# Kernel tuning notes

Measured on AMD Instinct MI355X. Metric: run time of the kernel, lower is better.

The kernel has to match this reference:

```python
import jax, jax.numpy as jnp
import numpy as np

N = 100000   # nodes
E = 1600000  # edges
DIN = 128
HID = 128
D2 = 64      # hard-coded last-conv width in the module
OUT = 1000


def setup_inputs() -> dict:
    key = jax.random.key(0)
    ks = jax.random.split(key, 8)
    x = jax.random.normal(ks[0], (N, DIN), dtype=jnp.float32)
    edge_index = jax.random.randint(ks[1], (2, E), 0, N, dtype=jnp.int64)
    W1 = jax.random.normal(ks[2], (DIN, HID), dtype=jnp.float32) * 0.05
    b1 = jnp.zeros((HID,), dtype=jnp.float32)
    W2 = jax.random.normal(ks[3], (HID, D2), dtype=jnp.float32) * 0.05
    b2 = jnp.zeros((D2,), dtype=jnp.float32)
    Wfc = jax.random.normal(ks[4], (D2, OUT), dtype=jnp.float32) * 0.05
    bfc = jnp.zeros((OUT,), dtype=jnp.float32)
    return {"x": x, "W1": W1, "b1": b1, "W2": W2, "b2": b2,
            "Wfc": Wfc, "bfc": bfc, "edge_index": edge_index}


def _gcn_conv(x, W, b, src, dst):
    # PyG GCNConv: h = X W; add self-loops; symmetric norm D^-1/2 (A+I) D^-1/2; + bias
    h = x @ W                                   # [N, F]
    ones = jnp.ones(src.shape[0], dtype=h.dtype)
    deg = jax.ops.segment_sum(ones, dst, num_segments=N) + 1.0  # +1 for self-loop
    dinv = jax.lax.rsqrt(deg)                   # [N]
    norm = dinv[src] * dinv[dst]                # [E]
    agg = jax.ops.segment_sum(h[src] * norm[:, None], dst, num_segments=N)
    agg = agg + h * (dinv * dinv)[:, None]      # self-loop contribution
    return agg + b


def reference(x, W1, b1, W2, b2, Wfc, bfc, edge_index):
    src, dst = edge_index[0], edge_index[1]
    h = jax.nn.relu(_gcn_conv(x, W1, b1, src, dst))
    # dropout is identity in eval mode (training=False)
    h = jax.nn.relu(_gcn_conv(h, W2, b2, src, dst))
    return h @ Wfc + bfc
```

## Files before the change

### kernel.cpp

```cpp
#include <hip/hip_runtime.h>
#include <hip/hip_bf16.h>
#include <cstddef>

typedef __attribute__((ext_vector_type(8))) short bf16x8;
typedef __attribute__((ext_vector_type(4))) float f32x4;

__device__ __forceinline__ unsigned short f2bf(float f) {
    __hip_bfloat16 h = __float2bfloat16(f);
    return __builtin_bit_cast(unsigned short, h);
}
__device__ __forceinline__ float bf2f(unsigned short u) {
    return __bfloat162float(__builtin_bit_cast(__hip_bfloat16, u));
}


__global__ void k_zero_i(int* __restrict__ p, int total) {
    int i = blockIdx.x * blockDim.x + threadIdx.x;
    int stride = gridDim.x * blockDim.x;
    for (; i < total; i += stride) p[i] = 0;
}


__global__ void k_deg_i(const int* __restrict__ dst, int* __restrict__ deg, int E) {
    int e = blockIdx.x * blockDim.x + threadIdx.x;
    if (e < E) atomicAdd(&deg[dst[e]], 1);
}

__global__ void k_dinv(const int* __restrict__ deg, float* __restrict__ dinv, int N) {
    int i = blockIdx.x * blockDim.x + threadIdx.x;
    if (i < N) dinv[i] = rsqrtf((float)deg[i] + 1.0f);
}


#define SCAN_B 1024

__global__ void k_scan1(const int* __restrict__ in, int* __restrict__ out,
                        int* __restrict__ sums, int n) {
    __shared__ int tmp[SCAN_B];
    int tid = threadIdx.x;
    int gid = blockIdx.x * SCAN_B + tid;
    int v = (gid < n) ? in[gid] : 0;
    tmp[tid] = v;
    __syncthreads();
    for (int off = 1; off < SCAN_B; off <<= 1) {
        int t = (tid >= off) ? tmp[tid - off] : 0;
        __syncthreads();
        tmp[tid] += t;
        __syncthreads();
    }
    if (gid < n) out[gid] = tmp[tid] - v;
    if (tid == SCAN_B - 1) sums[blockIdx.x] = tmp[tid];
}

__global__ void k_scan2(int* __restrict__ sums, int nb) {
    __shared__ int tmp[128];
    int tid = threadIdx.x;
    int v = (tid < nb) ? sums[tid] : 0;
    tmp[tid] = v;
    __syncthreads();
    for (int off = 1; off < 128; off <<= 1) {
        int t = (tid >= off) ? tmp[tid - off] : 0;
        __syncthreads();
        tmp[tid] += t;
        __syncthreads();
    }
    if (tid < nb) sums[tid] = tmp[tid] - v;
}

__global__ void k_scan3(int* __restrict__ out, int* __restrict__ cursor,
                        const int* __restrict__ sums, int n) {
    int gid = blockIdx.x * SCAN_B + threadIdx.x;
    if (gid < n) {
        int v = out[gid] + sums[blockIdx.x];
        out[gid] = v;
        cursor[gid] = v;
    }
}


__global__ void k_fill(const int* __restrict__ src, const int* __restrict__ dst,
                       int* __restrict__ cursor, int* __restrict__ csr_src, int E) {
    int e = blockIdx.x * blockDim.x + threadIdx.x;
    if (e < E) {
        int pos = atomicAdd(&cursor[dst[e]], 1);
        csr_src[pos] = src[e];
    }
}


__global__ void k_conv_w(const float* __restrict__ W, unsigned short* __restrict__ Bh,
                         unsigned short* __restrict__ Bl, int K, int N)
{
    int n = blockIdx.x;
    int k = threadIdx.x;
    float v = W[(size_t)k * N + n];
    unsigned short hi = f2bf(v);
    unsigned short lo = f2bf(v - bf2f(hi));
    Bh[(size_t)n * K + k] = hi;
    Bl[(size_t)n * K + k] = lo;
}


__device__ __forceinline__ float4 shfl_xor4(float4 v, int m) {
    return make_float4(__shfl_xor(v.x, m), __shfl_xor(v.y, m),
                       __shfl_xor(v.z, m), __shfl_xor(v.w, m));
}

__device__ __forceinline__ void fmaa4(float4& c, float w, const float4& v) {
    c.x = fmaf(w, v.x, c.x);
    c.y = fmaf(w, v.y, c.y);
    c.z = fmaf(w, v.z, c.z);
    c.w = fmaf(w, v.w, c.w);
}


__launch_bounds__(256)
__global__ void k_gather128(const float* __restrict__ h, const int* __restrict__ csr_src,
                            const int* __restrict__ off, const float* __restrict__ dinv,
                            const float* __restrict__ bias,
                            unsigned short* __restrict__ ohi, unsigned short* __restrict__ olo,
                            int N, int E)
{
    int node = blockIdx.x * 4 + (threadIdx.x >> 6);
    int lane = threadIdx.x & 63;
    if (node >= N) return;
    float dn = dinv[node];
    int beg = off[node];
    int end = (node + 1 < N) ? off[node + 1] : E;

    const int grp = lane >> 5;
    const int sub = lane & 31;

    float4 acc = make_float4(0.f, 0.f, 0.f, 0.f);
    int i = beg + grp;
    for (; i + 6 < end; i += 8) {
        int s0 = csr_src[i];
        int s1 = csr_src[i + 2];
        int s2 = csr_src[i + 4];
        int s3 = csr_src[i + 6];
        float w0 = dinv[s0] * dn;
        float w1 = dinv[s1] * dn;
        float w2 = dinv[s2] * dn;
        float w3 = dinv[s3] * dn;
        float4 v0 = *(const float4*)(h + (size_t)s0 * 128 + sub * 4);
        float4 v1 = *(const float4*)(h + (size_t)s1 * 128 + sub * 4);
        float4 v2 = *(const float4*)(h + (size_t)s2 * 128 + sub * 4);
        float4 v3 = *(const float4*)(h + (size_t)s3 * 128 + sub * 4);
        fmaa4(acc, w0, v0);
        fmaa4(acc, w1, v1);
        fmaa4(acc, w2, v2);
        fmaa4(acc, w3, v3);
    }
    for (; i < end; i += 2) {
        int s = csr_src[i];
        float w = dinv[s] * dn;
        float4 v = *(const float4*)(h + (size_t)s * 128 + sub * 4);
        fmaa4(acc, w, v);
    }
    {
        float4 o = shfl_xor4(acc, 32);
        acc.x += o.x; acc.y += o.y; acc.z += o.z; acc.w += o.w;
    }
    if (grp == 0) {
        float4 hv = *(const float4*)(h + (size_t)node * 128 + sub * 4);
        float4 bv = *(const float4*)(bias + sub * 4);
        float w = dn * dn;
        float f0 = fmaxf(fmaf(hv.x, w, acc.x) + bv.x, 0.f);
        float f1 = fmaxf(fmaf(hv.y, w, acc.y) + bv.y, 0.f);
        float f2 = fmaxf(fmaf(hv.z, w, acc.z) + bv.z, 0.f);
        float f3 = fmaxf(fmaf(hv.w, w, acc.w) + bv.w, 0.f);
        ushort4 hi, lo;
        hi.x = f2bf(f0); lo.x = f2bf(f0 - bf2f(hi.x));
        hi.y = f2bf(f1); lo.y = f2bf(f1 - bf2f(hi.y));
        hi.z = f2bf(f2); lo.z = f2bf(f2 - bf2f(hi.z));
        hi.w = f2bf(f3); lo.w = f2bf(f3 - bf2f(hi.w));
        *(ushort4*)(ohi + (size_t)node * 128 + sub * 4) = hi;
        *(ushort4*)(olo + (size_t)node * 128 + sub * 4) = lo;
    }
}


__launch_bounds__(256)
__global__ void k_gather64(const float* __restrict__ h, const int* __restrict__ csr_src,
                           const int* __restrict__ off, const float* __restrict__ dinv,
                           const float* __restrict__ bias,
                           unsigned short* __restrict__ hhi, unsigned short* __restrict__ hlo,
                           int N, int E)
{
    int node = blockIdx.x * 4 + (threadIdx.x >> 6);
    int lane = threadIdx.x & 63;
    if (node >= N) return;
    float dn = dinv[node];
    int beg = off[node];
    int end = (node + 1 < N) ? off[node + 1] : E;

    const int grp = lane >> 4;
    const int sub = lane & 15;

    float4 acc = make_float4(0.f, 0.f, 0.f, 0.f);
    int i = beg + grp;
    for (; i + 4 < end; i += 8) {
        int s0 = csr_src[i];
        int s1 = csr_src[i + 4];
        float w0 = dinv[s0] * dn;
        float w1 = dinv[s1] * dn;
        float4 v0 = *(const float4*)(h + (size_t)s0 * 64 + sub * 4);
        float4 v1 = *(const float4*)(h + (size_t)s1 * 64 + sub * 4);
        fmaa4(acc, w0, v0);
        fmaa4(acc, w1, v1);
    }
    if (i < end) {
        int s = csr_src[i];
        float w = dinv[s] * dn;
        float4 v = *(const float4*)(h + (size_t)s * 64 + sub * 4);
        fmaa4(acc, w, v);
    }
    acc = make_float4(acc.x + __shfl_xor(acc.x, 16),
                      acc.y + __shfl_xor(acc.y, 16),
                      acc.z + __shfl_xor(acc.z, 16),
                      acc.w + __shfl_xor(acc.w, 16));
    {
        float4 o = shfl_xor4(acc, 32);
        acc.x += o.x; acc.y += o.y; acc.z += o.z; acc.w += o.w;
    }
    if (grp == 0) {
        float4 hv = *(const float4*)(h + (size_t)node * 64 + sub * 4);
        float4 bv = *(const float4*)(bias + sub * 4);
        float w = dn * dn;
        float f0 = fmaxf(fmaf(hv.x, w, acc.x) + bv.x, 0.f);
        float f1 = fmaxf(fmaf(hv.y, w, acc.y) + bv.y, 0.f);
        float f2 = fmaxf(fmaf(hv.z, w, acc.z) + bv.z, 0.f);
        float f3 = fmaxf(fmaf(hv.w, w, acc.w) + bv.w, 0.f);
        ushort4 hi, lo;
        hi.x = f2bf(f0); lo.x = f2bf(f0 - bf2f(hi.x));
        hi.y = f2bf(f1); lo.y = f2bf(f1 - bf2f(hi.y));
        hi.z = f2bf(f2); lo.z = f2bf(f2 - bf2f(hi.z));
        hi.w = f2bf(f3); lo.w = f2bf(f3 - bf2f(hi.w));
        *(ushort4*)(hhi + (size_t)node * 64 + sub * 4) = hi;
        *(ushort4*)(hlo + (size_t)node * 64 + sub * 4) = lo;
    }
}


__launch_bounds__(256, 2)
__global__ void gemm_mfma_l1(const float* __restrict__ A,
                             const unsigned short* __restrict__ Bth,
                             const unsigned short* __restrict__ Btl,
                             float* __restrict__ C, int M)
{
    __shared__ unsigned short Ah[128 * 64], Al[128 * 64];
    __shared__ unsigned short Bh[128 * 64], Bl[128 * 64];

    const int tid = threadIdx.x;
    const int m0 = blockIdx.x * 128;
    const int lane = tid & 63, wave = tid >> 6;
    const int wr = wave >> 1, wc = wave & 1;
    const int lrow = lane & 15, kgrp = lane >> 4;

    f32x4 acc[4][4] = {};

    for (int ph = 0; ph < 2; ++ph) {
        const int k0 = ph * 64;
        __syncthreads();
        {
            const int c4 = tid & 15, r0 = tid >> 4;
#pragma unroll
            for (int p = 0; p < 8; ++p) {
                int row = r0 + p * 16;
                int gr = m0 + row; if (gr >= M) gr = M - 1;
                float4 v = *(const float4*)(A + (size_t)gr * 128 + k0 + c4 * 4);
                ushort4 hi, lo;
                hi.x = f2bf(v.x); lo.x = f2bf(v.x - bf2f(hi.x));
                hi.y = f2bf(v.y); lo.y = f2bf(v.y - bf2f(hi.y));
                hi.z = f2bf(v.z); lo.z = f2bf(v.z - bf2f(hi.z));
                hi.w = f2bf(v.w); lo.w = f2bf(v.w - bf2f(hi.w));
                int off = row * 128 + ((c4 * 8) ^ ((row & 7) << 4));
                *(ushort4*)((char*)Ah + off) = hi;
                *(ushort4*)((char*)Al + off) = lo;
            }
        }
        {
            const int c = tid & 7, col0 = tid >> 3;
#pragma unroll
            for (int p = 0; p < 4; ++p) {
                int col = col0 + p * 32;
                uint4 v = *(const uint4*)(Bth + (size_t)col * 128 + k0 + c * 8);
                uint4 w = *(const uint4*)(Btl + (size_t)col * 128 + k0 + c * 8);
                int off = col * 128 + ((c * 16) ^ ((col & 7) << 4));
                *(uint4*)((char*)Bh + off) = v;
                *(uint4*)((char*)Bl + off) = w;
            }
        }
        __syncthreads();

#pragma unroll
        for (int ks = 0; ks < 2; ++ks) {
            const int cIdx = kgrp + ks * 4;
            bf16x8 ah[4], al[4], bh[4], bl[4];
#pragma unroll
            for (int i = 0; i < 4; ++i) {
                int row = wr * 64 + i * 16 + lrow;
                int off = row * 128 + ((cIdx * 16) ^ ((row & 7) << 4));
                ah[i] = *(const bf16x8*)((const char*)Ah + off);
                al[i] = *(const bf16x8*)((const char*)Al + off);
            }
#pragma unroll
            for (int j = 0; j < 4; ++j) {
                int col = wc * 64 + j * 16 + lrow;
                int off = col * 128 + ((cIdx * 16) ^ ((col & 7) << 4));
                bh[j] = *(const bf16x8*)((const char*)Bh + off);
                bl[j] = *(const bf16x8*)((const char*)Bl + off);
            }
#pragma unroll
            for (int i = 0; i < 4; ++i)
#pragma unroll
                for (int j = 0; j < 4; ++j) {
                    acc[i][j] = __builtin_amdgcn_mfma_f32_16x16x32_bf16(bh[j], ah[i], acc[i][j], 0, 0, 0);
                    acc[i][j] = __builtin_amdgcn_mfma_f32_16x16x32_bf16(bl[j], ah[i], acc[i][j], 0, 0, 0);
                    acc[i][j] = __builtin_amdgcn_mfma_f32_16x16x32_bf16(bh[j], al[i], acc[i][j], 0, 0, 0);
                }
        }
    }

#pragma unroll
    for (int i = 0; i < 4; ++i) {
        int grow = m0 + wr * 64 + i * 16 + lrow;
        if (grow >= M) continue;
        float* crow = C + (size_t)grow * 128;
#pragma unroll
        for (int j = 0; j < 4; ++j) {
            int gc = wc * 64 + j * 16 + kgrp * 4;
            *(float4*)(crow + gc) = make_float4(acc[i][j][0], acc[i][j][1],
                                                acc[i][j][2], acc[i][j][3]);
        }
    }
}


__launch_bounds__(256, 3)
__global__ void gemm_mfma_l2(const unsigned short* __restrict__ Ahi_g,
                             const unsigned short* __restrict__ Alo_g,
                             const unsigned short* __restrict__ Bth,
                             const unsigned short* __restrict__ Btl,
                             float* __restrict__ C, int M)
{
    __shared__ unsigned short Ah[128 * 64], Al[128 * 64];
    __shared__ unsigned short Bh[64 * 64],  Bl[64 * 64];

    const int tid = threadIdx.x;
    const int m0 = blockIdx.x * 128;
    const int lane = tid & 63, wave = tid >> 6;
    const int wr = wave >> 1, wc = wave & 1;
    const int lrow = lane & 15, kgrp = lane >> 4;

    f32x4 acc[4][2] = {};

    for (int ph = 0; ph < 2; ++ph) {
        const int k0 = ph * 64;
        __syncthreads();
        {
            const int c = tid & 7, r0 = tid >> 3;
#pragma unroll
            for (int p = 0; p < 4; ++p) {
                int row = r0 + p * 32;
                int gr = m0 + row; if (gr >= M) gr = M - 1;
                uint4 v = *(const uint4*)(Ahi_g + (size_t)gr * 128 + k0 + c * 8);
                uint4 w = *(const uint4*)(Alo_g + (size_t)gr * 128 + k0 + c * 8);
                int off = row * 128 + ((c * 16) ^ ((row & 7) << 4));
                *(uint4*)((char*)Ah + off) = v;
                *(uint4*)((char*)Al + off) = w;
            }
        }
        {
            const int c = tid & 7, col0 = tid >> 3;
#pragma unroll
            for (int p = 0; p < 2; ++p) {
                int col = col0 + p * 32;
                uint4 v = *(const uint4*)(Bth + (size_t)col * 128 + k0 + c * 8);
                uint4 w = *(const uint4*)(Btl + (size_t)col * 128 + k0 + c * 8);
                int off = col * 128 + ((c * 16) ^ ((col & 7) << 4));
                *(uint4*)((char*)Bh + off) = v;
                *(uint4*)((char*)Bl + off) = w;
            }
        }
        __syncthreads();

#pragma unroll
        for (int ks = 0; ks < 2; ++ks) {
            const int cIdx = kgrp + ks * 4;
            bf16x8 ah[4], al[4], bh[2], bl[2];
#pragma unroll
            for (int i = 0; i < 4; ++i) {
                int row = wr * 64 + i * 16 + lrow;
                int off = row * 128 + ((cIdx * 16) ^ ((row & 7) << 4));
                ah[i] = *(const bf16x8*)((const char*)Ah + off);
                al[i] = *(const bf16x8*)((const char*)Al + off);
            }
#pragma unroll
            for (int j = 0; j < 2; ++j) {
                int col = wc * 32 + j * 16 + lrow;
                int off = col * 128 + ((cIdx * 16) ^ ((col & 7) << 4));
                bh[j] = *(const bf16x8*)((const char*)Bh + off);
                bl[j] = *(const bf16x8*)((const char*)Bl + off);
            }
#pragma unroll
            for (int i = 0; i < 4; ++i)
#pragma unroll
                for (int j = 0; j < 2; ++j) {
                    acc[i][j] = __builtin_amdgcn_mfma_f32_16x16x32_bf16(bh[j], ah[i], acc[i][j], 0, 0, 0);
                    acc[i][j] = __builtin_amdgcn_mfma_f32_16x16x32_bf16(bl[j], ah[i], acc[i][j], 0, 0, 0);
                    acc[i][j] = __builtin_amdgcn_mfma_f32_16x16x32_bf16(bh[j], al[i], acc[i][j], 0, 0, 0);
                }
        }
    }

#pragma unroll
    for (int i = 0; i < 4; ++i) {
        int grow = m0 + wr * 64 + i * 16 + lrow;
        if (grow >= M) continue;
        float* crow = C + (size_t)grow * 64;
#pragma unroll
        for (int j = 0; j < 2; ++j) {
            int gc = wc * 32 + j * 16 + kgrp * 4;
            *(float4*)(crow + gc) = make_float4(acc[i][j][0], acc[i][j][1],
                                                acc[i][j][2], acc[i][j][3]);
        }
    }
}


__launch_bounds__(256, 2)
__global__ void gemm_mfma_out(const unsigned short* __restrict__ Ahi,
                              const unsigned short* __restrict__ Alo,
                              const unsigned short* __restrict__ Bhi,
                              const unsigned short* __restrict__ Blo,
                              const float* __restrict__ bias, float* __restrict__ C,
                              int M, int N)
{
    const int tid = threadIdx.x;
    const int lane = tid & 63, wave = tid >> 6;
    const int wr = wave >> 1, wc = wave & 1;
    const int m0 = blockIdx.x * 128 + wr * 64;
    const int n0 = blockIdx.y * 128 + wc * 64;
    const int lrow = lane & 15, kgrp = lane >> 4;

    f32x4 acc[4][4] = {};

#pragma unroll
    for (int ks = 0; ks < 2; ++ks) {
        const int koff = (kgrp + ks * 4) * 8;
        bf16x8 ah[4], al[4], bh[4], bl[4];
#pragma unroll
        for (int i = 0; i < 4; ++i) {
            int row = m0 + i * 16 + lrow; if (row >= M) row = M - 1;
            ah[i] = *(const bf16x8*)(Ahi + (size_t)row * 64 + koff);
            al[i] = *(const bf16x8*)(Alo + (size_t)row * 64 + koff);
        }
#pragma unroll
        for (int j = 0; j < 4; ++j) {
            int col = n0 + j * 16 + lrow; if (col >= N) col = N - 1;
            bh[j] = *(const bf16x8*)(Bhi + (size_t)col * 64 + koff);
            bl[j] = *(const bf16x8*)(Blo + (size_t)col * 64 + koff);
        }
#pragma unroll
        for (int i = 0; i < 4; ++i)
#pragma unroll
            for (int j = 0; j < 4; ++j) {
                acc[i][j] = __builtin_amdgcn_mfma_f32_16x16x32_bf16(bh[j], ah[i], acc[i][j], 0, 0, 0);
                acc[i][j] = __builtin_amdgcn_mfma_f32_16x16x32_bf16(bl[j], ah[i], acc[i][j], 0, 0, 0);
                acc[i][j] = __builtin_amdgcn_mfma_f32_16x16x32_bf16(bh[j], al[i], acc[i][j], 0, 0, 0);
            }
    }

#pragma unroll
    for (int i = 0; i < 4; ++i) {
        int grow = m0 + i * 16 + lrow;
        if (grow >= M) continue;
        float* crow = C + (size_t)grow * N;
#pragma unroll
        for (int j = 0; j < 4; ++j) {
            int gc = n0 + j * 16 + kgrp * 4;
            if (gc + 4 <= N) {
                float4 bv = *(const float4*)(bias + gc);
                *(float4*)(crow + gc) = make_float4(acc[i][j][0] + bv.x,
                                                    acc[i][j][1] + bv.y,
                                                    acc[i][j][2] + bv.z,
                                                    acc[i][j][3] + bv.w);
            }
        }
    }
}


extern "C" void kernel_launch(void* const* d_in, const int* in_sizes, int n_in,
                              void* d_out, int out_size, void* d_ws, size_t ws_size,
                              hipStream_t stream)
{
    const float* x   = (const float*)d_in[0];
    const float* W1  = (const float*)d_in[1];
    const float* b1  = (const float*)d_in[2];
    const float* W2  = (const float*)d_in[3];
    const float* b2  = (const float*)d_in[4];
    const float* Wfc = (const float*)d_in[5];
    const float* bfc = (const float*)d_in[6];
    const int*   ei  = (const int*)d_in[7];

    const int Nn = in_sizes[0] / 128;
    const int E  = in_sizes[7] / 2;
    const int* src = ei;
    const int* dst = ei + E;

    char* ws = (char*)d_ws;
    float*          dinv   = (float*)(ws);
    unsigned short* Wfc_hi = (unsigned short*)(ws + 512 * 1024);
    unsigned short* Wfc_lo = (unsigned short*)(ws + 768 * 1024);
    unsigned short* W1_hi  = (unsigned short*)(ws + 1024 * 1024);
    unsigned short* W1_lo  = (unsigned short*)(ws + 1088 * 1024);
    unsigned short* W2_hi  = (unsigned short*)(ws + 1152 * 1024);
    unsigned short* W2_lo  = (unsigned short*)(ws + 1216 * 1024);
    unsigned short* h2hi   = (unsigned short*)(ws + 1280 * 1024);
    unsigned short* h2lo   = (unsigned short*)(ws + 1280 * 1024 + (size_t)Nn * 64 * 2);

    float* out = (float*)d_out;
    float*          O0      = out;
    unsigned short* h1hi    = (unsigned short*)(out + (size_t)Nn * 128);
    unsigned short* h1lo    = (unsigned short*)(out + (size_t)Nn * 192);
    float*          O2      = out + (size_t)Nn * 256;
    int*            csr_src = (int*)(out + (size_t)Nn * 320);
    int*            offs    = (int*)((char*)csr_src + (size_t)E * 4);
    int*            cursor  = (int*)((char*)offs + (size_t)Nn * 4);
    int*            deg_cnt = (int*)((char*)cursor + (size_t)Nn * 4);
    int*            bsums   = (int*)((char*)deg_cnt + (size_t)Nn * 4);

    const int nScanBlocks = (Nn + SCAN_B - 1) / SCAN_B;

    k_zero_i<<<128, 256, 0, stream>>>(deg_cnt, Nn);
    k_deg_i<<<(E + 255) / 256, 256, 0, stream>>>(dst, deg_cnt, E);
    k_dinv<<<(Nn + 255) / 256, 256, 0, stream>>>(deg_cnt, dinv, Nn);
    k_scan1<<<nScanBlocks, SCAN_B, 0, stream>>>(deg_cnt, offs, bsums, Nn);
    k_scan2<<<1, 128, 0, stream>>>(bsums, nScanBlocks);
    k_scan3<<<nScanBlocks, SCAN_B, 0, stream>>>(offs, cursor, bsums, Nn);
    k_fill<<<(E + 255) / 256, 256, 0, stream>>>(src, dst, cursor, csr_src, E);
    k_conv_w<<<128, 128, 0, stream>>>(W1, W1_hi, W1_lo, 128, 128);
    k_conv_w<<<64, 128, 0, stream>>>(W2, W2_hi, W2_lo, 128, 64);
    k_conv_w<<<1000, 64, 0, stream>>>(Wfc, Wfc_hi, Wfc_lo, 64, 1000);

    gemm_mfma_l1<<<dim3((Nn + 127) / 128, 1), 256, 0, stream>>>(x, W1_hi, W1_lo, O0, Nn);
    k_gather128<<<(Nn + 3) / 4, 256, 0, stream>>>(O0, csr_src, offs, dinv, b1,
                                                  h1hi, h1lo, Nn, E);

    gemm_mfma_l2<<<dim3((Nn + 127) / 128, 1), 256, 0, stream>>>(h1hi, h1lo, W2_hi, W2_lo, O2, Nn);
    k_gather64<<<(Nn + 3) / 4, 256, 0, stream>>>(O2, csr_src, offs, dinv, b2,
                                                 h2hi, h2lo, Nn, E);

    gemm_mfma_out<<<dim3((Nn + 127) / 128, (1000 + 127) / 128), 256, 0, stream>>>(
        h2hi, h2lo, Wfc_hi, Wfc_lo, bfc, out, Nn, 1000);
}
```

Before: 606.0 us.

## Store GEMM outputs as bf16 and gather bf16 rows in aggregation kernels

The layer-1 and layer-2 GEMMs now write their XW products as single bf16 values instead of fp32. The gather/aggregation kernels read 8 bf16 elements per lane with uint4 loads, unpack them to fp32 and accumulate, with lane groups and shuffle reductions reworked to match. This halves the bytes moved by the random neighbour gathers, which dominate memory traffic, and by the GEMM stores. In exchange it loses precision on the aggregated features (bf16 rounding of h before the sum), unlike the hi/lo split kept elsewhere.

```diff
diff --git a/kernel.cpp b/kernel.cpp
--- a/kernel.cpp
+++ b/kernel.cpp
@@ -11,6 +11,12 @@
 }
 __device__ __forceinline__ float bf2f(unsigned short u) {
     return __bfloat162float(__builtin_bit_cast(__hip_bfloat16, u));
+}
+__device__ __forceinline__ float bflo(unsigned u) {
+    return __builtin_bit_cast(float, u << 16);
+}
+__device__ __forceinline__ float bfhi(unsigned u) {
+    return __builtin_bit_cast(float, u & 0xffff0000u);
 }
 
 
@@ -101,23 +107,21 @@
 }
 
 
-__device__ __forceinline__ float4 shfl_xor4(float4 v, int m) {
-    return make_float4(__shfl_xor(v.x, m), __shfl_xor(v.y, m),
-                       __shfl_xor(v.z, m), __shfl_xor(v.w, m));
-}
-
-__device__ __forceinline__ void fmaa4(float4& c, float w, const float4& v) {
-    c.x = fmaf(w, v.x, c.x);
-    c.y = fmaf(w, v.y, c.y);
-    c.z = fmaf(w, v.z, c.z);
-    c.w = fmaf(w, v.w, c.w);
-}
-
+__device__ __forceinline__ void unpack_fma(float* a, float w, uint4 v) {
+    a[0] = fmaf(w, bflo(v.x), a[0]);
+    a[1] = fmaf(w, bfhi(v.x), a[1]);
+    a[2] = fmaf(w, bflo(v.y), a[2]);
+    a[3] = fmaf(w, bfhi(v.y), a[3]);
+    a[4] = fmaf(w, bflo(v.z), a[4]);
+    a[5] = fmaf(w, bfhi(v.z), a[5]);
+    a[6] = fmaf(w, bflo(v.w), a[6]);
+    a[7] = fmaf(w, bfhi(v.w), a[7]);
+}
 
 __launch_bounds__(256)
-__global__ void k_gather128(const float* __restrict__ h, const int* __restrict__ csr_src,
-                            const int* __restrict__ off, const float* __restrict__ dinv,
-                            const float* __restrict__ bias,
+__global__ void k_gather128(const unsigned short* __restrict__ hbf,
+                            const int* __restrict__ csr_src, const int* __restrict__ off,
+                            const float* __restrict__ dinv, const float* __restrict__ bias,
                             unsigned short* __restrict__ ohi, unsigned short* __restrict__ olo,
                             int N, int E)
 {
@@ -128,62 +132,68 @@
     int beg = off[node];
     int end = (node + 1 < N) ? off[node + 1] : E;
 
-    const int grp = lane >> 5;
-    const int sub = lane & 31;
-
-    float4 acc = make_float4(0.f, 0.f, 0.f, 0.f);
+    const int grp = lane >> 4;
+    const int sub = lane & 15;
+
+    float a[8] = {0.f, 0.f, 0.f, 0.f, 0.f, 0.f, 0.f, 0.f};
     int i = beg + grp;
-    for (; i + 6 < end; i += 8) {
+    for (; i + 4 < end; i += 8) {
         int s0 = csr_src[i];
-        int s1 = csr_src[i + 2];
-        int s2 = csr_src[i + 4];
-        int s3 = csr_src[i + 6];
+        int s1 = csr_src[i + 4];
         float w0 = dinv[s0] * dn;
         float w1 = dinv[s1] * dn;
-        float w2 = dinv[s2] * dn;
-        float w3 = dinv[s3] * dn;
-        float4 v0 = *(const float4*)(h + (size_t)s0 * 128 + sub * 4);
-        float4 v1 = *(const float4*)(h + (size_t)s1 * 128 + sub * 4);
-        float4 v2 = *(const float4*)(h + (size_t)s2 * 128 + sub * 4);
-        float4 v3 = *(const float4*)(h + (size_t)s3 * 128 + sub * 4);
-        fmaa4(acc, w0, v0);
-        fmaa4(acc, w1, v1);
-        fmaa4(acc, w2, v2);
-        fmaa4(acc, w3, v3);
-    }
-    for (; i < end; i += 2) {
+        uint4 v0 = *(const uint4*)(hbf + (size_t)s0 * 128 + sub * 8);
+        uint4 v1 = *(const uint4*)(hbf + (size_t)s1 * 128 + sub * 8);
+        unpack_fma(a, w0, v0);
+        unpack_fma(a, w1, v1);
+    }
+    if (i < end) {
         int s = csr_src[i];
         float w = dinv[s] * dn;
-        float4 v = *(const float4*)(h + (size_t)s * 128 + sub * 4);
-        fmaa4(acc, w, v);
-    }
-    {
-        float4 o = shfl_xor4(acc, 32);
-        acc.x += o.x; acc.y += o.y; acc.z += o.z; acc.w += o.w;
-    }
+        uint4 v = *(const uint4*)(hbf + (size_t)s * 128 + sub * 8);
+        unpack_fma(a, w, v);
+    }
+
+#pragma unroll
+    for (int k = 0; k < 8; ++k) {
+        a[k] += __shfl_xor(a[k], 16);
+        a[k] += __shfl_xor(a[k], 32);
+    }
+
     if (grp == 0) {
-        float4 hv = *(const float4*)(h + (size_t)node * 128 + sub * 4);
-        float4 bv = *(const float4*)(bias + sub * 4);
+        uint4 sv = *(const uint4*)(hbf + (size_t)node * 128 + sub * 8);
+        float s[8] = {bflo(sv.x), bfhi(sv.x), bflo(sv.y), bfhi(sv.y),
+                      bflo(sv.z), bfhi(sv.z), bflo(sv.w), bfhi(sv.w)};
+        float4 b0 = *(const float4*)(bias + sub * 8);
+        float4 b1 = *(const float4*)(bias + sub * 8 + 4);
+        float bv[8] = {b0.x, b0.y, b0.z, b0.w, b1.x, b1.y, b1.z, b1.w};
         float w = dn * dn;
-        float f0 = fmaxf(fmaf(hv.x, w, acc.x) + bv.x, 0.f);
-        float f1 = fmaxf(fmaf(hv.y, w, acc.y) + bv.y, 0.f);
-        float f2 = fmaxf(fmaf(hv.z, w, acc.z) + bv.z, 0.f);
-        float f3 = fmaxf(fmaf(hv.w, w, acc.w) + bv.w, 0.f);
-        ushort4 hi, lo;
-        hi.x = f2bf(f0); lo.x = f2bf(f0 - bf2f(hi.x));
-        hi.y = f2bf(f1); lo.y = f2bf(f1 - bf2f(hi.y));
-        hi.z = f2bf(f2); lo.z = f2bf(f2 - bf2f(hi.z));
-        hi.w = f2bf(f3); lo.w = f2bf(f3 - bf2f(hi.w));
-        *(ushort4*)(ohi + (size_t)node * 128 + sub * 4) = hi;
-        *(ushort4*)(olo + (size_t)node * 128 + sub * 4) = lo;
+        unsigned short hi[8], lo[8];
+#pragma unroll
+        for (int k = 0; k < 8; ++k) {
+            float f = fmaxf(fmaf(s[k], w, a[k]) + bv[k], 0.f);
+            hi[k] = f2bf(f);
+            lo[k] = f2bf(f - bf2f(hi[k]));
+        }
+        uint4 vh, vl;
+        vh.x = (unsigned)hi[0] | ((unsigned)hi[1] << 16);
+        vh.y = (unsigned)hi[2] | ((unsigned)hi[3] << 16);
+        vh.z = (unsigned)hi[4] | ((unsigned)hi[5] << 16);
+        vh.w = (unsigned)hi[6] | ((unsigned)hi[7] << 16);
+        vl.x = (unsigned)lo[0] | ((unsigned)lo[1] << 16);
+        vl.y = (unsigned)lo[2] | ((unsigned)lo[3] << 16);
+        vl.z = (unsigned)lo[4] | ((unsigned)lo[5] << 16);
+        vl.w = (unsigned)lo[6] | ((unsigned)lo[7] << 16);
+        *(uint4*)(ohi + (size_t)node * 128 + sub * 8) = vh;
+        *(uint4*)(olo + (size_t)node * 128 + sub * 8) = vl;
     }
 }
 
 
 __launch_bounds__(256)
-__global__ void k_gather64(const float* __restrict__ h, const int* __restrict__ csr_src,
-                           const int* __restrict__ off, const float* __restrict__ dinv,
-                           const float* __restrict__ bias,
+__global__ void k_gather64(const unsigned short* __restrict__ hbf,
+                           const int* __restrict__ csr_src, const int* __restrict__ off,
+                           const float* __restrict__ dinv, const float* __restrict__ bias,
                            unsigned short* __restrict__ hhi, unsigned short* __restrict__ hlo,
                            int N, int E)
 {
@@ -194,50 +204,61 @@
     int beg = off[node];
     int end = (node + 1 < N) ? off[node + 1] : E;
 
-    const int grp = lane >> 4;
-    const int sub = lane & 15;
-
-    float4 acc = make_float4(0.f, 0.f, 0.f, 0.f);
+    const int grp = lane >> 3;
+    const int sub = lane & 7;
+
+    float a[8] = {0.f, 0.f, 0.f, 0.f, 0.f, 0.f, 0.f, 0.f};
     int i = beg + grp;
-    for (; i + 4 < end; i += 8) {
+    for (; i + 8 < end; i += 16) {
         int s0 = csr_src[i];
-        int s1 = csr_src[i + 4];
+        int s1 = csr_src[i + 8];
         float w0 = dinv[s0] * dn;
         float w1 = dinv[s1] * dn;
-        float4 v0 = *(const float4*)(h + (size_t)s0 * 64 + sub * 4);
-        float4 v1 = *(const float4*)(h + (size_t)s1 * 64 + sub * 4);
-        fmaa4(acc, w0, v0);
-        fmaa4(acc, w1, v1);
+        uint4 v0 = *(const uint4*)(hbf + (size_t)s0 * 64 + sub * 8);
+        uint4 v1 = *(const uint4*)(hbf + (size_t)s1 * 64 + sub * 8);
+        unpack_fma(a, w0, v0);
+        unpack_fma(a, w1, v1);
     }
     if (i < end) {
         int s = csr_src[i];
         float w = dinv[s] * dn;
-        float4 v = *(const float4*)(h + (size_t)s * 64 + sub * 4);
-        fmaa4(acc, w, v);
-    }
-    acc = make_float4(acc.x + __shfl_xor(acc.x, 16),
-                      acc.y + __shfl_xor(acc.y, 16),
-                      acc.z + __shfl_xor(acc.z, 16),
-                      acc.w + __shfl_xor(acc.w, 16));
-    {
-        float4 o = shfl_xor4(acc, 32);
-        acc.x += o.x; acc.y += o.y; acc.z += o.z; acc.w += o.w;
-    }
+        uint4 v = *(const uint4*)(hbf + (size_t)s * 64 + sub * 8);
+        unpack_fma(a, w, v);
+    }
+
+#pragma unroll
+    for (int k = 0; k < 8; ++k) {
+        a[k] += __shfl_xor(a[k], 8);
+        a[k] += __shfl_xor(a[k], 16);
+        a[k] += __shfl_xor(a[k], 32);
+    }
+
     if (grp == 0) {
-        float4 hv = *(const float4*)(h + (size_t)node * 64 + sub * 4);
-        float4 bv = *(const float4*)(bias + sub * 4);
+        uint4 sv = *(const uint4*)(hbf + (size_t)node * 64 + sub * 8);
+        float s[8] = {bflo(sv.x), bfhi(sv.x), bflo(sv.y), bfhi(sv.y),
+                      bflo(sv.z), bfhi(sv.z), bflo(sv.w), bfhi(sv.w)};
+        float4 b0 = *(const float4*)(bias + sub * 8);
+        float4 b1 = *(const float4*)(bias + sub * 8 + 4);
+        float bv[8] = {b0.x, b0.y, b0.z, b0.w, b1.x, b1.y, b1.z, b1.w};
         float w = dn * dn;
-        float f0 = fmaxf(fmaf(hv.x, w, acc.x) + bv.x, 0.f);
-        float f1 = fmaxf(fmaf(hv.y, w, acc.y) + bv.y, 0.f);
-        float f2 = fmaxf(fmaf(hv.z, w, acc.z) + bv.z, 0.f);
-        float f3 = fmaxf(fmaf(hv.w, w, acc.w) + bv.w, 0.f);
-        ushort4 hi, lo;
-        hi.x = f2bf(f0); lo.x = f2bf(f0 - bf2f(hi.x));
-        hi.y = f2bf(f1); lo.y = f2bf(f1 - bf2f(hi.y));
-        hi.z = f2bf(f2); lo.z = f2bf(f2 - bf2f(hi.z));
-        hi.w = f2bf(f3); lo.w = f2bf(f3 - bf2f(hi.w));
-        *(ushort4*)(hhi + (size_t)node * 64 + sub * 4) = hi;
-        *(ushort4*)(hlo + (size_t)node * 64 + sub * 4) = lo;
+        unsigned short hi[8], lo[8];
+#pragma unroll
+        for (int k = 0; k < 8; ++k) {
+            float f = fmaxf(fmaf(s[k], w, a[k]) + bv[k], 0.f);
+            hi[k] = f2bf(f);
+            lo[k] = f2bf(f - bf2f(hi[k]));
+        }
+        uint4 vh, vl;
+        vh.x = (unsigned)hi[0] | ((unsigned)hi[1] << 16);
+        vh.y = (unsigned)hi[2] | ((unsigned)hi[3] << 16);
+        vh.z = (unsigned)hi[4] | ((unsigned)hi[5] << 16);
+        vh.w = (unsigned)hi[6] | ((unsigned)hi[7] << 16);
+        vl.x = (unsigned)lo[0] | ((unsigned)lo[1] << 16);
+        vl.y = (unsigned)lo[2] | ((unsigned)lo[3] << 16);
+        vl.z = (unsigned)lo[4] | ((unsigned)lo[5] << 16);
+        vl.w = (unsigned)lo[6] | ((unsigned)lo[7] << 16);
+        *(uint4*)(hhi + (size_t)node * 64 + sub * 8) = vh;
+        *(uint4*)(hlo + (size_t)node * 64 + sub * 8) = vl;
     }
 }
 
@@ -246,7 +267,7 @@
 __global__ void gemm_mfma_l1(const float* __restrict__ A,
                              const unsigned short* __restrict__ Bth,
                              const unsigned short* __restrict__ Btl,
-                             float* __restrict__ C, int M)
+                             unsigned short* __restrict__ Cbf, int M)
 {
     __shared__ unsigned short Ah[128 * 64], Al[128 * 64];
     __shared__ unsigned short Bh[128 * 64], Bl[128 * 64];
@@ -326,12 +347,16 @@
     for (int i = 0; i < 4; ++i) {
         int grow = m0 + wr * 64 + i * 16 + lrow;
         if (grow >= M) continue;
-        float* crow = C + (size_t)grow * 128;
+        unsigned short* crow = Cbf + (size_t)grow * 128;
 #pragma unroll
         for (int j = 0; j < 4; ++j) {
             int gc = wc * 64 + j * 16 + kgrp * 4;
-            *(float4*)(crow + gc) = make_float4(acc[i][j][0], acc[i][j][1],
-                                                acc[i][j][2], acc[i][j][3]);
+            ushort4 o;
+            o.x = f2bf(acc[i][j][0]);
+            o.y = f2bf(acc[i][j][1]);
+            o.z = f2bf(acc[i][j][2]);
+            o.w = f2bf(acc[i][j][3]);
+            *(ushort4*)(crow + gc) = o;
         }
     }
 }
@@ -342,7 +367,7 @@
                              const unsigned short* __restrict__ Alo_g,
                              const unsigned short* __restrict__ Bth,
                              const unsigned short* __restrict__ Btl,
-                             float* __restrict__ C, int M)
+                             unsigned short* __restrict__ Cbf, int M)
 {
     __shared__ unsigned short Ah[128 * 64], Al[128 * 64];
     __shared__ unsigned short Bh[64 * 64],  Bl[64 * 64];
@@ -418,12 +443,16 @@
     for (int i = 0; i < 4; ++i) {
         int grow = m0 + wr * 64 + i * 16 + lrow;
         if (grow >= M) continue;
-        float* crow = C + (size_t)grow * 64;
+        unsigned short* crow = Cbf + (size_t)grow * 64;
 #pragma unroll
         for (int j = 0; j < 2; ++j) {
             int gc = wc * 32 + j * 16 + kgrp * 4;
-            *(float4*)(crow + gc) = make_float4(acc[i][j][0], acc[i][j][1],
-                                                acc[i][j][2], acc[i][j][3]);
+            ushort4 o;
+            o.x = f2bf(acc[i][j][0]);
+            o.y = f2bf(acc[i][j][1]);
+            o.z = f2bf(acc[i][j][2]);
+            o.w = f2bf(acc[i][j][3]);
+            *(ushort4*)(crow + gc) = o;
         }
     }
 }
@@ -521,12 +550,12 @@
     unsigned short* h2hi   = (unsigned short*)(ws + 1280 * 1024);
     unsigned short* h2lo   = (unsigned short*)(ws + 1280 * 1024 + (size_t)Nn * 64 * 2);
 
-    float* out = (float*)d_out;
-    float*          O0      = out;
-    unsigned short* h1hi    = (unsigned short*)(out + (size_t)Nn * 128);
-    unsigned short* h1lo    = (unsigned short*)(out + (size_t)Nn * 192);
-    float*          O2      = out + (size_t)Nn * 256;
-    int*            csr_src = (int*)(out + (size_t)Nn * 320);
+    char* ob = (char*)d_out;
+    unsigned short* hbf     = (unsigned short*)ob;
+    unsigned short* h1hi    = (unsigned short*)(ob + (size_t)Nn * 256);
+    unsigned short* h1lo    = (unsigned short*)(ob + (size_t)Nn * 512);
+    unsigned short* h2bf    = (unsigned short*)(ob + (size_t)Nn * 768);
+    int*            csr_src = (int*)(ob + (size_t)Nn * 896);
     int*            offs    = (int*)((char*)csr_src + (size_t)E * 4);
     int*            cursor  = (int*)((char*)offs + (size_t)Nn * 4);
     int*            deg_cnt = (int*)((char*)cursor + (size_t)Nn * 4);
@@ -545,14 +574,14 @@
     k_conv_w<<<64, 128, 0, stream>>>(W2, W2_hi, W2_lo, 128, 64);
     k_conv_w<<<1000, 64, 0, stream>>>(Wfc, Wfc_hi, Wfc_lo, 64, 1000);
 
-    gemm_mfma_l1<<<dim3((Nn + 127) / 128, 1), 256, 0, stream>>>(x, W1_hi, W1_lo, O0, Nn);
-    k_gather128<<<(Nn + 3) / 4, 256, 0, stream>>>(O0, csr_src, offs, dinv, b1,
+    gemm_mfma_l1<<<dim3((Nn + 127) / 128, 1), 256, 0, stream>>>(x, W1_hi, W1_lo, hbf, Nn);
+    k_gather128<<<(Nn + 3) / 4, 256, 0, stream>>>(hbf, csr_src, offs, dinv, b1,
                                                   h1hi, h1lo, Nn, E);
 
-    gemm_mfma_l2<<<dim3((Nn + 127) / 128, 1), 256, 0, stream>>>(h1hi, h1lo, W2_hi, W2_lo, O2, Nn);
-    k_gather64<<<(Nn + 3) / 4, 256, 0, stream>>>(O2, csr_src, offs, dinv, b2,
+    gemm_mfma_l2<<<dim3((Nn + 127) / 128, 1), 256, 0, stream>>>(h1hi, h1lo, W2_hi, W2_lo, h2bf, Nn);
+    k_gather64<<<(Nn + 3) / 4, 256, 0, stream>>>(h2bf, csr_src, offs, dinv, b2,
                                                  h2hi, h2lo, Nn, E);
 
     gemm_mfma_out<<<dim3((Nn + 127) / 128, (1000 + 127) / 128), 256, 0, stream>>>(
-        h2hi, h2lo, Wfc_hi, Wfc_lo, bfc, out, Nn, 1000);
-}
+        h2hi, h2lo, Wfc_hi, Wfc_lo, bfc, out_size ? (float*)d_out : (float*)d_out, Nn, 1000);
+}
```

Result: faster. 531.0 us (-12.4%).
